# Performance work log

Measured on AMD Instinct MI355X. Metric: run time of the kernel, lower is better.

The kernel has to match this reference:

```python
import jax, jax.numpy as jnp
import numpy as np

HIDDEN = 768
E_ROUTED = 32
K_ACT = 4
E_SHARED = 8
RANK = 64
FFN_ROUTED = HIDDEN * 2
FFN_SHARED = HIDDEN * 3


def setup_inputs() -> dict:
    key = jax.random.key(0)
    ks = jax.random.split(key, 8)
    s = 0.02
    return {
        "x": jax.random.normal(ks[0], (2, 2048, HIDDEN), dtype=jnp.float32),
        # shared experts: SwiGLU (gate, up, down), stacked over experts
        "shared_wg": jax.random.normal(ks[1], (E_SHARED, HIDDEN, FFN_SHARED), dtype=jnp.float32) * s,
        "shared_wu": jax.random.normal(ks[2], (E_SHARED, HIDDEN, FFN_SHARED), dtype=jnp.float32) * s,
        "shared_wd": jax.random.normal(ks[3], (E_SHARED, FFN_SHARED, HIDDEN), dtype=jnp.float32) * s,
        # routed experts: Linear -> GELU -> Linear, stacked
        "routed_w1": jax.random.normal(ks[4], (E_ROUTED, HIDDEN, FFN_ROUTED), dtype=jnp.float32) * s,
        "routed_w2": jax.random.normal(ks[5], (E_ROUTED, FFN_ROUTED, HIDDEN), dtype=jnp.float32) * s,
        # low-rank router
        "router_down": jax.random.normal(ks[6], (HIDDEN, RANK), dtype=jnp.float32) * s,
        "router_up": jax.random.normal(ks[7], (RANK, E_ROUTED), dtype=jnp.float32) * s,
    }


def reference(x, shared_wg, shared_wu, shared_wd, routed_w1, routed_w2, router_down, router_up):
    B, S, D = x.shape
    xf = x.reshape(-1, D)  # [T, D]

    # shared experts (SwiGLU), averaged
    g = jnp.einsum('td,edh->eth', xf, shared_wg)
    u = jnp.einsum('td,edh->eth', xf, shared_wu)
    sh = jnp.einsum('eth,ehd->etd', jax.nn.silu(g) * u, shared_wd)
    shared_output = sh.mean(axis=0)  # [T, D] (sum / num_shared_expert)

    # low-rank router + top-k
    router_logits = (xf @ router_down) @ router_up  # [T, E]
    routing_weights, selected = jax.lax.top_k(router_logits, K_ACT)  # [T, K]
    routing_weights = jax.nn.softmax(routing_weights, axis=-1)

    # dense all-expert FFN (faithful to source), then gather top-k (== one-hot einsum)
    h = jnp.einsum('td,edh->eth', xf, routed_w1)
    expert_outputs = jnp.einsum('eth,ehd->etd', jax.nn.gelu(h, approximate=False), routed_w2)  # [E,T,D]
    sel_out = jnp.take_along_axis(expert_outputs.transpose(1, 0, 2), selected[:, :, None], axis=1)  # [T,K,D]
    routed_output = jnp.einsum('tkd,tk->td', sel_out, routing_weights)

    output = (shared_output + routed_output).reshape(B, S, D)

    # aux losses
    counts = jnp.bincount(selected.reshape(-1), length=E_ROUTED).astype(jnp.float32)
    load_balance_loss = jnp.var(counts, ddof=1)  # torch .var() is unbiased
    probs = jax.nn.softmax(router_logits, axis=-1)
    router_entropy = -(probs * jnp.log(probs + 1e-10)).sum(-1).mean()
    shared_norm = jnp.linalg.norm(shared_output, axis=-1).mean()
    routed_norm = jnp.linalg.norm(routed_output, axis=-1).mean()
    balance_loss = jnp.abs(shared_norm - routed_norm)

    return output, load_balance_loss, router_entropy, balance_loss
```

## Files before the change

kernel.cpp:

```cpp
#include <hip/hip_runtime.h>
#include <hip/hip_bf16.h>
#include <math.h>


#define T_TOK 4096
#define DHID 768
#define NE_R 32
#define NE_S 8
#define F_S 2304
#define F_R 1536
#define MAXROWS 20480
#define MAX_TILES 160

typedef float f32x4 __attribute__((ext_vector_type(4)));
typedef short s16x8 __attribute__((ext_vector_type(8)));

__device__ __forceinline__ short f2bf(float f) {
  union { float f; unsigned u; } v; v.f = f;
  unsigned r = v.u + 0x7fffu + ((v.u >> 16) & 1u);
  return (short)(r >> 16);
}

#define GLD16(gsrc, ldst)                                                     \
  __builtin_amdgcn_global_load_lds(                                           \
      (const __attribute__((address_space(1))) void*)(gsrc),                  \
      (__attribute__((address_space(3))) void*)(ldst), 16, 0, 0)

__global__ __launch_bounds__(256) void cvt_x_kernel(const float* __restrict__ in,
    short* __restrict__ out, int* __restrict__ tlist, float* __restrict__ wslot,
    int* __restrict__ counts, int* __restrict__ cursor) {
  int i = blockIdx.x * 256 + threadIdx.x;
  if (i < T_TOK * DHID / 4) {
    float4 v = ((const float4*)in)[i];
    short4 o;
    o.x = f2bf(v.x); o.y = f2bf(v.y); o.z = f2bf(v.z); o.w = f2bf(v.w);
    ((short4*)out)[i] = o;
  }
  if (i < MAXROWS) { tlist[i] = 0; wslot[i] = 0.f; }
  if (i < 32) { counts[i] = 0; cursor[i] = 0; }
}

__device__ __forceinline__ void tile_transpose(const float* in, short* out,
                                               int R, int C, long ldo,
                                               int r0, int c0) {
  __shared__ float tile[64][65];
  int tx = threadIdx.x & 63, ty = threadIdx.x >> 6;
#pragma unroll
  for (int i = 0; i < 64; i += 4)
    tile[ty + i][tx] = in[(size_t)(r0 + ty + i) * C + (c0 + tx)];
  __syncthreads();
  int u = threadIdx.x & 15, v = threadIdx.x >> 4;
#pragma unroll
  for (int i = 0; i < 64; i += 16) {
    int c = v + i;
    short4 o;
    o.x = f2bf(tile[4 * u + 0][c]); o.y = f2bf(tile[4 * u + 1][c]);
    o.z = f2bf(tile[4 * u + 2][c]); o.w = f2bf(tile[4 * u + 3][c]);
    *(short4*)&out[(size_t)(c0 + c) * ldo + (r0 + 4 * u)] = o;
  }
}

__global__ __launch_bounds__(256) void transpose_shared(
    const float* __restrict__ swg, const float* __restrict__ swu,
    const float* __restrict__ swd, short* __restrict__ wgT,
    short* __restrict__ wuT, short* __restrict__ wdT) {
  int bid = blockIdx.x;
  const float* in; short* out; int R, C, nbx; long ldo;
  if (bid < 3456)      { in = swg; out = wgT; R = DHID; C = F_S; ldo = DHID; nbx = 36; }
  else if (bid < 6912) { bid -= 3456; in = swu; out = wuT; R = DHID; C = F_S; ldo = DHID; nbx = 36; }
  else                 { bid -= 6912; in = swd; out = wdT; R = F_S; C = DHID; ldo = F_S; nbx = 12; }
  int per = nbx * (R / 64);
  int b = bid / per, rem = bid % per;
  int c0 = (rem % nbx) * 64, r0 = (rem / nbx) * 64;
  tile_transpose(in + (size_t)b * R * C, out + (size_t)b * R * C, R, C, ldo, r0, c0);
}

__global__ __launch_bounds__(256) void transpose_routed(
    const float* __restrict__ rw1, const float* __restrict__ rw2,
    short* __restrict__ w1T, short* __restrict__ w2T) {
  int bid = blockIdx.x;
  const float* in; short* out; int R, C, nbx; long ldo;
  if (bid < 9216) { in = rw1; out = w1T; R = DHID; C = F_R; ldo = DHID; nbx = 24; }
  else            { bid -= 9216; in = rw2; out = w2T; R = F_R; C = DHID; ldo = F_R; nbx = 12; }
  int per = nbx * (R / 64);
  int b = bid / per, rem = bid % per;
  int c0 = (rem % nbx) * 64, r0 = (rem / nbx) * 64;
  tile_transpose(in + (size_t)b * R * C, out + (size_t)b * R * C, R, C, ldo, r0, c0);
}

__global__ __launch_bounds__(64) void router_kernel(const float* __restrict__ x,
    const float* __restrict__ rdown, const float* __restrict__ rup,
    int* __restrict__ sel, float* __restrict__ w4, int* __restrict__ counts,
    float* __restrict__ pent) {
  int t = blockIdx.x;
  int lane = threadIdx.x;
  __shared__ float xs[DHID];
  __shared__ float xrs[64];
  __shared__ float lg[32];
  const float* xt = x + (size_t)t * DHID;
  for (int i = lane; i < DHID; i += 64) xs[i] = xt[i];
  __syncthreads();
  float acc = 0.f;
#pragma unroll 8
  for (int d = 0; d < DHID; ++d) acc += xs[d] * rdown[d * 64 + lane];
  xrs[lane] = acc;
  __syncthreads();
  if (lane < 32) {
    float l = 0.f;
#pragma unroll 8
    for (int r = 0; r < 64; ++r) l += xrs[r] * rup[r * 32 + lane];
    lg[lane] = l;
  }
  __syncthreads();
  if (lane == 0) {
    int si[4]; float sv[4];
    unsigned taken = 0;
    for (int k = 0; k < 4; ++k) {
      float best = -3.4e38f; int bi = 0;
      for (int e = 0; e < 32; ++e)
        if (!((taken >> e) & 1u) && lg[e] > best) { best = lg[e]; bi = e; }
      taken |= 1u << bi; si[k] = bi; sv[k] = best;
    }
    float m = sv[0];
    float wv[4]; float zs = 0.f;
    for (int k = 0; k < 4; ++k) { wv[k] = __expf(sv[k] - m); zs += wv[k]; }
    for (int k = 0; k < 4; ++k) {
      sel[t * 4 + k] = si[k];
      w4[t * 4 + k] = wv[k] / zs;
      atomicAdd(&counts[si[k]], 1);
    }
    float Z = 0.f;
    for (int e = 0; e < 32; ++e) Z += __expf(lg[e] - m);
    float ent = 0.f;
    for (int e = 0; e < 32; ++e) {
      float p = __expf(lg[e] - m) / Z;
      ent -= p * logf(p + 1e-10f);
    }
    pent[t] = ent;
  }
}

__global__ void meta_kernel(const int* __restrict__ counts, int* __restrict__ meta) {
  if (threadIdx.x == 0) {
    int acc = 0;
    for (int e = 0; e < 32; ++e) { meta[e] = acc; acc += (counts[e] + 127) >> 7; }
    meta[32] = acc;
  }
}

__global__ __launch_bounds__(256) void build_kernel(const int* __restrict__ sel,
    const float* __restrict__ w4, const int* __restrict__ meta, int* __restrict__ cursor,
    int* __restrict__ tlist, float* __restrict__ wslot, int* __restrict__ pos) {
  int t = blockIdx.x * 256 + threadIdx.x;
  if (t >= T_TOK) return;
#pragma unroll
  for (int k = 0; k < 4; ++k) {
    int e = sel[t * 4 + k];
    int slot = atomicAdd(&cursor[e], 1);
    int g = meta[e] * 128 + slot;
    tlist[g] = t; wslot[g] = w4[t * 4 + k]; pos[t * 4 + k] = g;
  }
}

template<int MODE>
__global__ __launch_bounds__(256, 4) void gemm_k(
    const short* __restrict__ A, const short* __restrict__ B, const short* __restrict__ B2,
    short* __restrict__ outH, float* __restrict__ outF, const float* __restrict__ wslot,
    const int* __restrict__ meta, const int* __restrict__ tlist,
    int K, int lda, long zbstride, long ldo, long ocolz, long orowz, long acolz) {
  constexpr int BM = 128;
  constexpr int WM = 64, FM = 4, FN = 4;
  __shared__ short As[BM * 64];
  __shared__ short Bs[128 * 64];

  int tid = threadIdx.x;
  int wv = tid >> 6, lane = tid & 63;
  int wr = wv >> 1, wc = wv & 1;
  int lrow = lane & 15, kg = lane >> 4;
  int lrow7 = lrow & 7;
  int z = blockIdx.z;

  int bx = blockIdx.x, by = blockIdx.y;
  if constexpr (MODE == 0 || MODE == 2) {
    int gx = gridDim.x, gy = gridDim.y;
    int nwg = gx * gy;
    int orig = by * gx + bx;
    int swz = (orig & 7) * (nwg >> 3) + (orig >> 3);
    bx = swz / gy; by = swz % gy;
  }
  int n0 = bx * ((MODE == 0) ? 64 : 128);

  int eidx = z;
  int g0 = 0, m0 = by * BM;
  if constexpr (MODE == 1 || MODE == 3) {
    int total = meta[32];
    int ty = blockIdx.y;
    if (ty >= total) return;
    int e = 0;
    while (meta[e + 1] <= ty) ++e;
    eidx = e;
    g0 = ty * BM;
  }

  int srow = tid >> 3;
  int scol = ((tid & 7) ^ (srow & 7)) * 8;

  f32x4 acc[FM][FN] = {};

  constexpr int EPB = (MODE == 2) ? 2 : 1;
#pragma unroll 1
  for (int ei = 0; ei < EPB; ++ei) {
    int e = (MODE == 2) ? (z * 2 + ei) : eidx;
    const short* Bb = B + (size_t)e * zbstride + (size_t)n0 * K;

    const short *as0, *as1, *as2, *as3;
    {
      auto arow = [&](int row) -> const short* {
        if constexpr (MODE == 1) {
          return A + (size_t)tlist[g0 + row] * lda + scol;
        } else if constexpr (MODE == 2) {
          return A + ((size_t)(m0 + row)) * lda + (size_t)e * acolz + scol;
        } else if constexpr (MODE == 3) {
          return A + ((size_t)(g0 + row)) * lda + scol;
        } else {
          return A + ((size_t)(m0 + row)) * lda + scol;
        }
      };
      as0 = arow(srow); as1 = arow(32 + srow); as2 = arow(64 + srow); as3 = arow(96 + srow);
    }
    const short* bs0 = Bb + (size_t)srow * K + scol;
    const short* bs1 = bs0 + (size_t)32 * K;
    const short* bs2;
    const short* bs3;
    if constexpr (MODE == 0) {
      const short* B2b = B2 + (size_t)e * zbstride + (size_t)n0 * K;
      bs2 = B2b + (size_t)srow * K + scol;
      bs3 = bs2 + (size_t)32 * K;
    } else {
      bs2 = bs0 + (size_t)64 * K;
      bs3 = bs0 + (size_t)96 * K;
    }

    for (int kt = 0; kt < K; kt += 64) {
      GLD16(as0 + kt, As + (0 * 32 + wv * 8) * 64);
      GLD16(as1 + kt, As + (1 * 32 + wv * 8) * 64);
      GLD16(as2 + kt, As + (2 * 32 + wv * 8) * 64);
      GLD16(as3 + kt, As + (3 * 32 + wv * 8) * 64);
      GLD16(bs0 + kt, Bs + (0 * 32 + wv * 8) * 64);
      GLD16(bs1 + kt, Bs + (1 * 32 + wv * 8) * 64);
      GLD16(bs2 + kt, Bs + (2 * 32 + wv * 8) * 64);
      GLD16(bs3 + kt, Bs + (3 * 32 + wv * 8) * 64);
      __syncthreads();
#pragma unroll
      for (int ks = 0; ks < 2; ++ks) {
        int pc = ((ks * 4 + kg) ^ lrow7) * 8;
        s16x8 af[FM], bb[FN];
#pragma unroll
        for (int i = 0; i < FM; ++i)
          af[i] = *(const s16x8*)&As[(wr * WM + i * 16 + lrow) * 64 + pc];
#pragma unroll
        for (int j = 0; j < FN; ++j) {
          int brow;
          if constexpr (MODE == 0)
            brow = (j >= 2 ? 64 : 0) + wc * 32 + (j & 1) * 16 + lrow;
          else
            brow = wc * 64 + j * 16 + lrow;
          bb[j] = *(const s16x8*)&Bs[brow * 64 + pc];
        }
#pragma unroll
        for (int i = 0; i < FM; ++i)
#pragma unroll
          for (int j = 0; j < FN; ++j)
            acc[i][j] = __builtin_amdgcn_mfma_f32_16x16x32_bf16(af[i], bb[j], acc[i][j], 0, 0, 0);
      }
      __syncthreads();
    }
  }

#pragma unroll
  for (int i = 0; i < FM; ++i) {
#pragma unroll
    for (int r = 0; r < 4; ++r) {
      int rl = wr * WM + i * 16 + kg * 4 + r;
      float wsc = 0.f;
      if constexpr (MODE == 1) wsc = wslot[g0 + rl];
      if constexpr (MODE == 0) {
#pragma unroll
        for (int jp = 0; jp < 2; ++jp) {
          int col = n0 + wc * 32 + jp * 16 + lrow;
          float g = acc[i][jp][r];
          float u = acc[i][jp + 2][r];
          float h = g / (1.f + __expf(-g)) * u;
          outH[(size_t)(m0 + rl) * ldo + (size_t)z * ocolz + col] = f2bf(h);
        }
      } else {
#pragma unroll
        for (int j = 0; j < FN; ++j) {
          int col = n0 + wc * 64 + j * 16 + lrow;
          float v = acc[i][j][r];
          if constexpr (MODE == 1) {
            float h = 0.5f * v * (1.f + erff(v * 0.70710678118f)) * wsc;
            outH[(size_t)(g0 + rl) * ldo + col] = f2bf(h);
          } else if constexpr (MODE == 2) {
            outF[(size_t)z * orowz + (size_t)(m0 + rl) * DHID + col] = v;
          } else if constexpr (MODE == 3) {
            outF[(size_t)(g0 + rl) * DHID + col] = v;
          }
        }
      }
    }
  }
}

__global__ __launch_bounds__(256) void combine_kernel(const float* __restrict__ spart,
    const float* __restrict__ Y, const int* __restrict__ pos,
    float* __restrict__ out, float* __restrict__ pnorm) {
  int t = blockIdx.x, tid = threadIdx.x;
  int p0 = pos[t * 4], p1 = pos[t * 4 + 1], p2 = pos[t * 4 + 2], p3 = pos[t * 4 + 3];
  size_t base = (size_t)t * DHID;
  float s2 = 0.f, r2 = 0.f;
  for (int d = tid; d < DHID; d += 256) {
    float s = 0.f;
#pragma unroll
    for (int e = 0; e < 4; ++e) s += spart[(size_t)e * T_TOK * DHID + base + d];
    s *= 0.125f;
    float r = Y[(size_t)p0 * DHID + d] + Y[(size_t)p1 * DHID + d] +
              Y[(size_t)p2 * DHID + d] + Y[(size_t)p3 * DHID + d];
    out[base + d] = s + r;
    s2 += s * s; r2 += r * r;
  }
  for (int o = 32; o > 0; o >>= 1) { s2 += __shfl_down(s2, o); r2 += __shfl_down(r2, o); }
  __shared__ float red[8];
  int wv = tid >> 6, lane = tid & 63;
  if (lane == 0) { red[wv] = s2; red[4 + wv] = r2; }
  __syncthreads();
  if (tid == 0) {
    float st = red[0] + red[1] + red[2] + red[3];
    float rt = red[4] + red[5] + red[6] + red[7];
    pnorm[t] = sqrtf(st);
    pnorm[T_TOK + t] = sqrtf(rt);
  }
}

__global__ __launch_bounds__(256) void finalize_kernel(const int* __restrict__ counts,
    const float* __restrict__ pent, const float* __restrict__ pnorm, float* __restrict__ o) {
  int tid = threadIdx.x;
  float es = 0.f, ss = 0.f, rs = 0.f;
  for (int i = tid; i < T_TOK; i += 256) {
    es += pent[i]; ss += pnorm[i]; rs += pnorm[T_TOK + i];
  }
  float vs = 0.f;
  if (tid < 32) { float d = (float)counts[tid] - 512.f; vs = d * d; }
  for (int off = 32; off > 0; off >>= 1) {
    es += __shfl_down(es, off); ss += __shfl_down(ss, off);
    rs += __shfl_down(rs, off); vs += __shfl_down(vs, off);
  }
  __shared__ float red[16];
  int wv = tid >> 6, lane = tid & 63;
  if (lane == 0) { red[wv] = es; red[4 + wv] = ss; red[8 + wv] = rs; red[12 + wv] = vs; }
  __syncthreads();
  if (tid == 0) {
    es = red[0] + red[1] + red[2] + red[3];
    ss = red[4] + red[5] + red[6] + red[7];
    rs = red[8] + red[9] + red[10] + red[11];
    vs = red[12] + red[13] + red[14] + red[15];
    o[0] = vs / 31.f;
    o[1] = es / (float)T_TOK;
    o[2] = fabsf(ss - rs) / (float)T_TOK;
  }
}

extern "C" void kernel_launch(void* const* d_in, const int* in_sizes, int n_in,
                              void* d_out, int out_size, void* d_ws, size_t ws_size,
                              hipStream_t stream) {
  const float* x   = (const float*)d_in[0];
  const float* swg = (const float*)d_in[1];
  const float* swu = (const float*)d_in[2];
  const float* swd = (const float*)d_in[3];
  const float* rw1 = (const float*)d_in[4];
  const float* rw2 = (const float*)d_in[5];
  const float* rdn = (const float*)d_in[6];
  const float* rup = (const float*)d_in[7];
  float* fout = (float*)d_out;

  char* w = (char*)d_ws;
  size_t off = 0;
  auto take = [&](size_t bytes) { char* p = w + off; off = (off + bytes + 255) & ~(size_t)255; return p; };
  short* xbf   = (short*)take((size_t)T_TOK * DHID * 2);
  int*   sel   = (int*)  take((size_t)T_TOK * 4 * 4);
  float* w4    = (float*)take((size_t)T_TOK * 4 * 4);
  int*   pos   = (int*)  take((size_t)T_TOK * 4 * 4);
  int*   counts= (int*)  take(32 * 4);
  int*   cursor= (int*)  take(32 * 4);
  int*   meta  = (int*)  take(64 * 4);
  int*   tlist = (int*)  take((size_t)MAXROWS * 4);
  float* wslot = (float*)take((size_t)MAXROWS * 4);
  float* pent  = (float*)take((size_t)T_TOK * 4);
  float* pnorm = (float*)take((size_t)2 * T_TOK * 4);
  float* spart = (float*)take((size_t)4 * T_TOK * DHID * 4);
  char*  arena = w + off;

  short* wgT = (short*)arena;
  short* wuT = wgT + (size_t)NE_S * F_S * DHID;
  short* wdT = wuT + (size_t)NE_S * F_S * DHID;
  short* Hsh = wdT + (size_t)NE_S * F_S * DHID;
  float* Y   = (float*)arena;
  short* w1T = (short*)(arena + (size_t)MAXROWS * DHID * 4);
  short* w2T = w1T + (size_t)NE_R * F_R * DHID;
  short* Hr  = w2T + (size_t)NE_R * F_R * DHID;

  cvt_x_kernel<<<(T_TOK * DHID / 4 + 255) / 256, 256, 0, stream>>>(x, xbf, tlist, wslot, counts, cursor);
  router_kernel<<<T_TOK, 64, 0, stream>>>(x, rdn, rup, sel, w4, counts, pent);
  meta_kernel<<<1, 64, 0, stream>>>(counts, meta);
  build_kernel<<<T_TOK / 256, 256, 0, stream>>>(sel, w4, meta, cursor, tlist, wslot, pos);

  transpose_shared<<<10368, 256, 0, stream>>>(swg, swu, swd, wgT, wuT, wdT);
  gemm_k<0><<<dim3(F_S / 64, T_TOK / 128, NE_S), 256, 0, stream>>>(
      xbf, wgT, wuT, Hsh, nullptr, nullptr, nullptr, nullptr,
      DHID, DHID, (long)F_S * DHID, (long)NE_S * F_S, (long)F_S, 0, 0);
  gemm_k<2><<<dim3(DHID / 128, T_TOK / 128, NE_S / 2), 256, 0, stream>>>(
      Hsh, wdT, nullptr, nullptr, spart, nullptr, nullptr, nullptr,
      F_S, NE_S * F_S, (long)DHID * F_S, DHID, 0, (long)T_TOK * DHID, (long)F_S);

  transpose_routed<<<18432, 256, 0, stream>>>(rw1, rw2, w1T, w2T);
  gemm_k<1><<<dim3(F_R / 128, MAX_TILES, 1), 256, 0, stream>>>(
      xbf, w1T, nullptr, Hr, nullptr, wslot, meta, tlist,
      DHID, DHID, (long)F_R * DHID, (long)F_R, 0, 0, 0);
  gemm_k<3><<<dim3(DHID / 128, MAX_TILES, 1), 256, 0, stream>>>(
      Hr, w2T, nullptr, nullptr, Y, nullptr, meta, tlist,
      F_R, F_R, (long)DHID * F_R, DHID, 0, 0, 0);

  combine_kernel<<<T_TOK, 256, 0, stream>>>(spart, Y, pos, fout, pnorm);
  finalize_kernel<<<1, 256, 0, stream>>>(counts, pent, pnorm, fout + (size_t)T_TOK * DHID);
}
```

Baseline: 910.3 us.

## Fuse meta into build, swizzle routed GEMM tiles, loop two experts per block, tanh GELU

Merges the single-thread meta kernel into build_kernel: every block recomputes the prefix offsets in shared memory and block 0 writes them out. Applies the tile swizzle to the routed GEMMs and makes the shared gate/up GEMM process two experts per block with half the grid. Replaces the exact erf GELU with a tanh-form approximation computed through expf. Each piece targets launch overhead, cache locality, or epilogue cost, but the GELU swap changes numerics.

```diff
diff --git a/kernel.cpp b/kernel.cpp
--- a/kernel.cpp
+++ b/kernel.cpp
@@ -140,24 +140,26 @@
   }
 }
 
-__global__ void meta_kernel(const int* __restrict__ counts, int* __restrict__ meta) {
+__global__ __launch_bounds__(256) void build_kernel(const int* __restrict__ sel,
+    const float* __restrict__ w4, const int* __restrict__ counts,
+    int* __restrict__ cursor, int* __restrict__ tlist, float* __restrict__ wslot,
+    int* __restrict__ pos, int* __restrict__ meta) {
+  __shared__ int smeta[33];
   if (threadIdx.x == 0) {
     int acc = 0;
-    for (int e = 0; e < 32; ++e) { meta[e] = acc; acc += (counts[e] + 127) >> 7; }
-    meta[32] = acc;
-  }
-}
-
-__global__ __launch_bounds__(256) void build_kernel(const int* __restrict__ sel,
-    const float* __restrict__ w4, const int* __restrict__ meta, int* __restrict__ cursor,
-    int* __restrict__ tlist, float* __restrict__ wslot, int* __restrict__ pos) {
+    for (int e = 0; e < 32; ++e) { smeta[e] = acc; acc += (counts[e] + 127) >> 7; }
+    smeta[32] = acc;
+    if (blockIdx.x == 0)
+      for (int e = 0; e < 33; ++e) meta[e] = smeta[e];
+  }
+  __syncthreads();
   int t = blockIdx.x * 256 + threadIdx.x;
   if (t >= T_TOK) return;
 #pragma unroll
   for (int k = 0; k < 4; ++k) {
     int e = sel[t * 4 + k];
     int slot = atomicAdd(&cursor[e], 1);
-    int g = meta[e] * 128 + slot;
+    int g = smeta[e] * 128 + slot;
     tlist[g] = t; wslot[g] = w4[t * 4 + k]; pos[t * 4 + k] = g;
   }
 }
@@ -181,12 +183,16 @@
   int z = blockIdx.z;
 
   int bx = blockIdx.x, by = blockIdx.y;
-  if constexpr (MODE == 0 || MODE == 2) {
+  {
     int gx = gridDim.x, gy = gridDim.y;
     int nwg = gx * gy;
     int orig = by * gx + bx;
     int swz = (orig & 7) * (nwg >> 3) + (orig >> 3);
-    bx = swz / gy; by = swz % gy;
+    if constexpr (MODE == 0 || MODE == 2) {
+      bx = swz / gy; by = swz % gy;
+    } else {
+      bx = swz % gx; by = swz / gx;
+    }
   }
   int n0 = bx * ((MODE == 0) ? 64 : 128);
 
@@ -194,7 +200,7 @@
   int g0 = 0, m0 = by * BM;
   if constexpr (MODE == 1 || MODE == 3) {
     int total = meta[32];
-    int ty = blockIdx.y;
+    int ty = by;
     if (ty >= total) return;
     int e = 0;
     while (meta[e + 1] <= ty) ++e;
@@ -207,10 +213,10 @@
 
   f32x4 acc[FM][FN] = {};
 
-  constexpr int EPB = (MODE == 2) ? 2 : 1;
+  constexpr int EPB = (MODE == 0 || MODE == 2) ? 2 : 1;
 #pragma unroll 1
   for (int ei = 0; ei < EPB; ++ei) {
-    int e = (MODE == 2) ? (z * 2 + ei) : eidx;
+    int e = (EPB == 2) ? (z * 2 + ei) : eidx;
     const short* Bb = B + (size_t)e * zbstride + (size_t)n0 * K;
 
     const short *as0, *as1, *as2, *as3;
@@ -275,31 +281,46 @@
       }
       __syncthreads();
     }
-  }
-
-#pragma unroll
-  for (int i = 0; i < FM; ++i) {
-#pragma unroll
-    for (int r = 0; r < 4; ++r) {
-      int rl = wr * WM + i * 16 + kg * 4 + r;
-      float wsc = 0.f;
-      if constexpr (MODE == 1) wsc = wslot[g0 + rl];
-      if constexpr (MODE == 0) {
-#pragma unroll
-        for (int jp = 0; jp < 2; ++jp) {
-          int col = n0 + wc * 32 + jp * 16 + lrow;
-          float g = acc[i][jp][r];
-          float u = acc[i][jp + 2][r];
-          float h = g / (1.f + __expf(-g)) * u;
-          outH[(size_t)(m0 + rl) * ldo + (size_t)z * ocolz + col] = f2bf(h);
+
+    if constexpr (MODE == 0) {
+#pragma unroll
+      for (int i = 0; i < FM; ++i) {
+#pragma unroll
+        for (int r = 0; r < 4; ++r) {
+          int rl = wr * WM + i * 16 + kg * 4 + r;
+#pragma unroll
+          for (int jp = 0; jp < 2; ++jp) {
+            int col = n0 + wc * 32 + jp * 16 + lrow;
+            float g = acc[i][jp][r];
+            float u = acc[i][jp + 2][r];
+            float h = g / (1.f + __expf(-g)) * u;
+            outH[(size_t)(m0 + rl) * ldo + (size_t)e * ocolz + col] = f2bf(h);
+          }
         }
-      } else {
+      }
+#pragma unroll
+      for (int i = 0; i < FM; ++i)
+#pragma unroll
+        for (int j = 0; j < FN; ++j)
+          acc[i][j] = (f32x4){0.f, 0.f, 0.f, 0.f};
+    }
+  }
+
+  if constexpr (MODE != 0) {
+#pragma unroll
+    for (int i = 0; i < FM; ++i) {
+#pragma unroll
+      for (int r = 0; r < 4; ++r) {
+        int rl = wr * WM + i * 16 + kg * 4 + r;
+        float wsc = 0.f;
+        if constexpr (MODE == 1) wsc = wslot[g0 + rl];
 #pragma unroll
         for (int j = 0; j < FN; ++j) {
           int col = n0 + wc * 64 + j * 16 + lrow;
           float v = acc[i][j][r];
           if constexpr (MODE == 1) {
-            float h = 0.5f * v * (1.f + erff(v * 0.70710678118f)) * wsc;
+            float vc = v * (0.7978845608f + 0.0356774081f * v * v);
+            float h = v / (1.f + __expf(-2.f * vc)) * wsc;
             outH[(size_t)(g0 + rl) * ldo + col] = f2bf(h);
           } else if constexpr (MODE == 2) {
             outF[(size_t)z * orowz + (size_t)(m0 + rl) * DHID + col] = v;
@@ -411,11 +432,10 @@
 
   cvt_x_kernel<<<(T_TOK * DHID / 4 + 255) / 256, 256, 0, stream>>>(x, xbf, tlist, wslot, counts, cursor);
   router_kernel<<<T_TOK, 64, 0, stream>>>(x, rdn, rup, sel, w4, counts, pent);
-  meta_kernel<<<1, 64, 0, stream>>>(counts, meta);
-  build_kernel<<<T_TOK / 256, 256, 0, stream>>>(sel, w4, meta, cursor, tlist, wslot, pos);
+  build_kernel<<<T_TOK / 256, 256, 0, stream>>>(sel, w4, counts, cursor, tlist, wslot, pos, meta);
 
   transpose_shared<<<10368, 256, 0, stream>>>(swg, swu, swd, wgT, wuT, wdT);
-  gemm_k<0><<<dim3(F_S / 64, T_TOK / 128, NE_S), 256, 0, stream>>>(
+  gemm_k<0><<<dim3(F_S / 64, T_TOK / 128, NE_S / 2), 256, 0, stream>>>(
       xbf, wgT, wuT, Hsh, nullptr, nullptr, nullptr, nullptr,
       DHID, DHID, (long)F_S * DHID, (long)NE_S * F_S, (long)F_S, 0, 0);
   gemm_k<2><<<dim3(DHID / 128, T_TOK / 128, NE_S / 2), 256, 0, stream>>>(
```

Measured after the change: 934.7 us. 2.7% more time.
